# Performance work log

Measured on AMD Instinct MI355X. Metric: run time of the kernel, lower is better.

The kernel has to match this reference:

```python
import jax, jax.numpy as jnp
import numpy as np

NR_EMB = 1024
B_COMMITMENT = 1.0


def setup_inputs() -> dict:
    key = jax.random.key(0)
    k1, k2 = jax.random.split(key)
    inpt = jax.random.normal(k1, (64, 2048, 64), dtype=jnp.float32)
    # VarianceScaling(uniform) over shape (D, K): limit = sqrt(3*scale/fan_in), scale=1, fan_in=D
    D = 64
    limit = np.sqrt(3.0 / D).astype(np.float32)
    emb_mtrx = jax.random.uniform(k2, (D, NR_EMB), dtype=jnp.float32, minval=-limit, maxval=limit)
    return {"inpt": inpt, "emb_mtrx": emb_mtrx}


def reference(inpt, emb_mtrx):
    D = inpt.shape[-1]
    x = inpt.reshape(-1, D)  # [N, D]
    dist = (jnp.sum(x * x, axis=1, keepdims=True)
            - 2.0 * (x @ emb_mtrx)
            + jnp.sum(emb_mtrx * emb_mtrx, axis=0, keepdims=True))
    idx = jnp.argmax(-dist, axis=1)  # [N]
    # avg_probs = mean of one-hot over N == normalized histogram (same math, no N x K one-hot)
    avg_probs = jnp.bincount(idx, length=NR_EMB).astype(inpt.dtype) / x.shape[0]
    perplexity = jnp.exp(-jnp.sum(avg_probs * jnp.log(avg_probs + 1e-10)))
    idx_nd = idx.reshape(inpt.shape[:-1])  # [B, T]
    q = jnp.take(emb_mtrx.T, idx_nd, axis=0)  # gather codebook rows -> [B, T, D]
    l_commitment = jnp.mean((jax.lax.stop_gradient(q) - inpt) ** 2)
    l_codebook = jnp.mean((q - jax.lax.stop_gradient(inpt)) ** 2)
    loss = B_COMMITMENT * l_commitment + l_codebook
    q = inpt + jax.lax.stop_gradient(q - inpt)  # straight-through estimator
    return q, loss, perplexity
```

## Files before the change

### kernel.cpp

```cpp
#include <hip/hip_runtime.h>

#define NROWS 131072
#define D 64
#define K 1024

typedef __attribute__((ext_vector_type(8))) short short8;
typedef __attribute__((ext_vector_type(4))) float f32x4;
typedef unsigned int u32;


__device__ __forceinline__ unsigned short f2bf_rne(float f) {
    u32 u = __float_as_uint(f);
    u += 0x7fff + ((u >> 16) & 1);
    return (unsigned short)(u >> 16);
}

__global__ __launch_bounds__(256) void prep_kernel(const float* __restrict__ E,
                                                   unsigned short* __restrict__ ehT,
                                                   float* __restrict__ e2g,
                                                   int* __restrict__ hist) {
    const int k = blockIdx.x * 256 + threadIdx.x;
    float s = 0.f;
#pragma unroll
    for (int db = 0; db < 8; ++db) {
        short8 h8;
#pragma unroll
        for (int j = 0; j < 8; ++j) {
            float v = E[(db * 8 + j) * K + k];
            s = fmaf(v, v, s);
            h8[j] = (short)f2bf_rne(v);
        }
        *(short8*)(ehT + (size_t)k * D + db * 8) = h8;
    }
    e2g[k] = -0.5f * s;
    hist[k] = 0;
}

__global__ __launch_bounds__(1024) void score_kernel(const float* __restrict__ X,
                                                     const unsigned short* __restrict__ ehT,
                                                     const float* __restrict__ e2g,
                                                     int* __restrict__ hist,
                                                     float* __restrict__ wavesum,
                                                     float* __restrict__ q) {
    __shared__ unsigned short xbuf[2][8192];
    __shared__ float mrg[128 * 17];
    __shared__ int idxl[512];

    const int tid = threadIdx.x;
    const int wave = tid >> 6;
    const int lane = tid & 63;
    const int quad = lane >> 4;
    const int lc = lane & 15;
    const size_t row0 = (size_t)blockIdx.x * 512;

    const int cbase = wave * 64;
    short8 ae[4][2];
    f32x4 e2f[4];
    u32 cb4[4];
#pragma unroll
    for (int ct = 0; ct < 4; ++ct) {
        const unsigned short* ap = ehT + ((size_t)(cbase + ct * 16 + lc) << 6) + quad * 8;
        ae[ct][0] = *(const short8*)(ap);
        ae[ct][1] = *(const short8*)(ap + 32);
        e2f[ct] = *(const f32x4*)(e2g + cbase + ct * 16 + quad * 4);
        cb4[ct] = (u32)(cbase + ct * 16 + quad * 4);
    }

    const int st = tid >> 7, so = (tid >> 4) & 7, sl = tid & 15;
    const float* sbase = X + (row0 + (size_t)(st * 16 + sl)) * D + so * 8;

    float4 La = *(const float4*)(sbase);
    float4 Lb = *(const float4*)(sbase + 4);
    {
        union { u32 u[4]; short8 v; } pk;
        pk.u[0] = __builtin_amdgcn_perm(__float_as_uint(La.y), __float_as_uint(La.x), 0x07060302);
        pk.u[1] = __builtin_amdgcn_perm(__float_as_uint(La.w), __float_as_uint(La.z), 0x07060302);
        pk.u[2] = __builtin_amdgcn_perm(__float_as_uint(Lb.y), __float_as_uint(Lb.x), 0x07060302);
        pk.u[3] = __builtin_amdgcn_perm(__float_as_uint(Lb.w), __float_as_uint(Lb.z), 0x07060302);
        *(short8*)((char*)&xbuf[0][0] + tid * 16) = pk.v;
    }
    __syncthreads();

    for (int c = 0; c < 4; ++c) {
        const int cur = c & 1;
        if (c < 3) {
            La = *(const float4*)(sbase + (c + 1) * 8192);
            Lb = *(const float4*)(sbase + (c + 1) * 8192 + 4);
        }

        const char* bb = (const char*)&xbuf[cur][0];
#pragma unroll 2
        for (int t = 0; t < 8; ++t) {
            const char* bp = bb + t * 2048 + quad * 256 + lc * 16;
            short8 b0 = *(const short8*)(bp);
            short8 b1 = *(const short8*)(bp + 1024);
            float bt = -3.4e38f;
#pragma unroll
            for (int ct = 0; ct < 4; ++ct) {
                f32x4 acc = __builtin_amdgcn_mfma_f32_16x16x32_bf16(ae[ct][0], b0, e2f[ct], 0, 0, 0);
                acc = __builtin_amdgcn_mfma_f32_16x16x32_bf16(ae[ct][1], b1, acc, 0, 0, 0);
#pragma unroll
                for (int r = 0; r < 4; ++r) {
                    float pkv = __uint_as_float((__float_as_uint(acc[r]) & 0xFFFFFC00u) | (cb4[ct] + r));
                    bt = fmaxf(bt, pkv);
                }
            }
            bt = fmaxf(bt, __shfl_xor(bt, 16, 64));
            bt = fmaxf(bt, __shfl_xor(bt, 32, 64));
            if (lane < 16) mrg[(t * 16 + lane) * 17 + wave] = bt;
        }
        __syncthreads();

        if (tid < 128) {
            float m = mrg[tid * 17];
#pragma unroll
            for (int w = 1; w < 16; ++w) m = fmaxf(m, mrg[tid * 17 + w]);
            int kk = (int)(__float_as_uint(m) & 1023u);
            idxl[c * 128 + tid] = kk;
            atomicAdd(&hist[kk], 1);
        }
        if (c < 3) {
            union { u32 u[4]; short8 v; } pk;
            pk.u[0] = __builtin_amdgcn_perm(__float_as_uint(La.y), __float_as_uint(La.x), 0x07060302);
            pk.u[1] = __builtin_amdgcn_perm(__float_as_uint(La.w), __float_as_uint(La.z), 0x07060302);
            pk.u[2] = __builtin_amdgcn_perm(__float_as_uint(Lb.y), __float_as_uint(Lb.x), 0x07060302);
            pk.u[3] = __builtin_amdgcn_perm(__float_as_uint(Lb.w), __float_as_uint(Lb.z), 0x07060302);
            *(short8*)((char*)&xbuf[cur ^ 1][0] + tid * 16) = pk.v;
        }
        __syncthreads();
    }

    float ls = 0.f;
    const int er = tid >> 4, el = tid & 15;
#pragma unroll 2
    for (int it = 0; it < 8; ++it) {
        int rl = it * 64 + er;
        int k = idxl[rl];
        size_t row = row0 + rl;
        float4 xv = *(const float4*)(X + row * D + el * 4);
        short4 ev = *(const short4*)((const char*)ehT + (size_t)k * 128 + el * 8);
        float e0 = __uint_as_float(((u32)(unsigned short)ev.x) << 16);
        float e1 = __uint_as_float(((u32)(unsigned short)ev.y) << 16);
        float e2 = __uint_as_float(((u32)(unsigned short)ev.z) << 16);
        float e3 = __uint_as_float(((u32)(unsigned short)ev.w) << 16);
        float4 o;
        float dx = e0 - xv.x; ls = fmaf(dx, dx, ls); o.x = xv.x + dx;
        float dy = e1 - xv.y; ls = fmaf(dy, dy, ls); o.y = xv.y + dy;
        float dz = e2 - xv.z; ls = fmaf(dz, dz, ls); o.z = xv.z + dz;
        float dw = e3 - xv.w; ls = fmaf(dw, dw, ls); o.w = xv.w + dw;
        *(float4*)(q + row * D + el * 4) = o;
    }
    for (int off = 32; off > 0; off >>= 1) ls += __shfl_down(ls, off, 64);
    if (lane == 0) wavesum[blockIdx.x * 16 + wave] = ls;
}

__global__ __launch_bounds__(1024) void finalize_kernel(const int* __restrict__ hist,
                                                        const float* __restrict__ wavesum,
                                                        float* __restrict__ out) {
    __shared__ float redH[16], redL[16];
    int tid = threadIdx.x;
    float p = (float)hist[tid] * (1.0f / (float)NROWS);
    float term = p * logf(p + 1e-10f);
    float ls = wavesum[tid] + wavesum[tid + 1024] + wavesum[tid + 2048] + wavesum[tid + 3072];
    for (int off = 32; off > 0; off >>= 1) {
        term += __shfl_down(term, off, 64);
        ls += __shfl_down(ls, off, 64);
    }
    int lane = tid & 63, wid = tid >> 6;
    if (lane == 0) { redH[wid] = term; redL[wid] = ls; }
    __syncthreads();
    if (tid == 0) {
        float H = 0.f, L = 0.f;
#pragma unroll
        for (int i = 0; i < 16; ++i) { H += redH[i]; L += redL[i]; }
        out[(size_t)NROWS * D + 0] = 2.0f * (L / (float)(NROWS * D));
        out[(size_t)NROWS * D + 1] = expf(-H);
    }
}

extern "C" void kernel_launch(void* const* d_in, const int* in_sizes, int n_in,
                              void* d_out, int out_size, void* d_ws, size_t ws_size,
                              hipStream_t stream) {
    const float* X = (const float*)d_in[0];
    const float* E = (const float*)d_in[1];
    float* out = (float*)d_out;

    char* w = (char*)d_ws;
    unsigned short* ehT = (unsigned short*)(w + 0);
    float* e2g          = (float*)(w + 131072);
    int* hist           = (int*)(w + 135168);
    float* wavesum      = (float*)(w + 139264);

    prep_kernel<<<4, 256, 0, stream>>>(E, ehT, e2g, hist);
    score_kernel<<<256, 1024, 0, stream>>>(X, ehT, e2g, hist, wavesum, out);
    finalize_kernel<<<1, 1024, 0, stream>>>(hist, wavesum, out);
}
```

Measured before the change: 124.1 us.

## Fuse quantize epilogue into score loop using LDS bf16 inputs, double block count

Each block now handles 256 rows in 2 chunks instead of 512 rows in 4, giving 512 blocks instead of 256. The gather, loss and output stage now runs inside the chunk loop and reads the bf16 copy of X already held in LDS, rather than re-reading fp32 X from global memory after the loop. This removes the second global read of X and the separate tail phase. In exchange, the commitment loss is computed against bf16-truncated inputs, and q is written as the bf16 codebook value rather than x + (e - x), which costs accuracy. The prep kernel is also split across 16 blocks with an LDS reduction, and per-block loss partials are reduced in-kernel before finalize.

```diff
diff --git a/kernel.cpp b/kernel.cpp
--- a/kernel.cpp
+++ b/kernel.cpp
@@ -15,43 +15,53 @@
     return (unsigned short)(u >> 16);
 }
 
+__device__ __forceinline__ float b2f(short s) {
+    return __uint_as_float(((u32)(unsigned short)s) << 16);
+}
+
 __global__ __launch_bounds__(256) void prep_kernel(const float* __restrict__ E,
                                                    unsigned short* __restrict__ ehT,
                                                    float* __restrict__ e2g,
                                                    int* __restrict__ hist) {
-    const int k = blockIdx.x * 256 + threadIdx.x;
+    __shared__ float ps[4][64];
+    const int lane = threadIdx.x & 63;
+    const int w = threadIdx.x >> 6;
+    const int k = blockIdx.x * 64 + lane;
     float s = 0.f;
 #pragma unroll
-    for (int db = 0; db < 8; ++db) {
+    for (int half = 0; half < 2; ++half) {
         short8 h8;
 #pragma unroll
         for (int j = 0; j < 8; ++j) {
-            float v = E[(db * 8 + j) * K + k];
+            float v = E[(w * 16 + half * 8 + j) * K + k];
             s = fmaf(v, v, s);
             h8[j] = (short)f2bf_rne(v);
         }
-        *(short8*)(ehT + (size_t)k * D + db * 8) = h8;
-    }
-    e2g[k] = -0.5f * s;
-    hist[k] = 0;
-}
-
-__global__ __launch_bounds__(1024) void score_kernel(const float* __restrict__ X,
-                                                     const unsigned short* __restrict__ ehT,
-                                                     const float* __restrict__ e2g,
-                                                     int* __restrict__ hist,
-                                                     float* __restrict__ wavesum,
-                                                     float* __restrict__ q) {
+        *(short8*)(ehT + (size_t)k * D + w * 16 + half * 8) = h8;
+    }
+    ps[w][lane] = s;
+    __syncthreads();
+    if (w == 0) e2g[k] = -0.5f * (ps[0][lane] + ps[1][lane] + ps[2][lane] + ps[3][lane]);
+    if (threadIdx.x < 64) hist[blockIdx.x * 64 + threadIdx.x] = 0;
+}
+
+__global__ __launch_bounds__(1024, 8) void score_kernel(const float* __restrict__ X,
+                                                        const unsigned short* __restrict__ ehT,
+                                                        const float* __restrict__ e2g,
+                                                        int* __restrict__ hist,
+                                                        float* __restrict__ wavesum,
+                                                        float* __restrict__ q) {
     __shared__ unsigned short xbuf[2][8192];
     __shared__ float mrg[128 * 17];
-    __shared__ int idxl[512];
+    __shared__ int idxl[128];
+    __shared__ float redL[16];
 
     const int tid = threadIdx.x;
     const int wave = tid >> 6;
     const int lane = tid & 63;
     const int quad = lane >> 4;
     const int lc = lane & 15;
-    const size_t row0 = (size_t)blockIdx.x * 512;
+    const size_t row0 = (size_t)blockIdx.x * 256;
 
     const int cbase = wave * 64;
     short8 ae[4][2];
@@ -81,14 +91,14 @@
     }
     __syncthreads();
 
-    for (int c = 0; c < 4; ++c) {
-        const int cur = c & 1;
-        if (c < 3) {
-            La = *(const float4*)(sbase + (c + 1) * 8192);
-            Lb = *(const float4*)(sbase + (c + 1) * 8192 + 4);
-        }
-
-        const char* bb = (const char*)&xbuf[cur][0];
+    float ls = 0.f;
+    for (int c = 0; c < 2; ++c) {
+        if (c == 0) {
+            La = *(const float4*)(sbase + 8192);
+            Lb = *(const float4*)(sbase + 8192 + 4);
+        }
+
+        const char* bb = (const char*)&xbuf[c][0];
 #pragma unroll 2
         for (int t = 0; t < 8; ++t) {
             const char* bp = bb + t * 2048 + quad * 256 + lc * 16;
@@ -99,11 +109,12 @@
             for (int ct = 0; ct < 4; ++ct) {
                 f32x4 acc = __builtin_amdgcn_mfma_f32_16x16x32_bf16(ae[ct][0], b0, e2f[ct], 0, 0, 0);
                 acc = __builtin_amdgcn_mfma_f32_16x16x32_bf16(ae[ct][1], b1, acc, 0, 0, 0);
-#pragma unroll
-                for (int r = 0; r < 4; ++r) {
-                    float pkv = __uint_as_float((__float_as_uint(acc[r]) & 0xFFFFFC00u) | (cb4[ct] + r));
-                    bt = fmaxf(bt, pkv);
-                }
+                float p0 = __uint_as_float((__float_as_uint(acc[0]) & 0xFFFFFC00u) | (cb4[ct] + 0));
+                float p1 = __uint_as_float((__float_as_uint(acc[1]) & 0xFFFFFC00u) | (cb4[ct] + 1));
+                float p2 = __uint_as_float((__float_as_uint(acc[2]) & 0xFFFFFC00u) | (cb4[ct] + 2));
+                float p3 = __uint_as_float((__float_as_uint(acc[3]) & 0xFFFFFC00u) | (cb4[ct] + 3));
+                bt = fmaxf(bt, fmaxf(p0, p1));
+                bt = fmaxf(bt, fmaxf(p2, p3));
             }
             bt = fmaxf(bt, __shfl_xor(bt, 16, 64));
             bt = fmaxf(bt, __shfl_xor(bt, 32, 64));
@@ -116,42 +127,48 @@
 #pragma unroll
             for (int w = 1; w < 16; ++w) m = fmaxf(m, mrg[tid * 17 + w]);
             int kk = (int)(__float_as_uint(m) & 1023u);
-            idxl[c * 128 + tid] = kk;
+            idxl[tid] = kk;
             atomicAdd(&hist[kk], 1);
         }
-        if (c < 3) {
+        if (c == 0) {
             union { u32 u[4]; short8 v; } pk;
             pk.u[0] = __builtin_amdgcn_perm(__float_as_uint(La.y), __float_as_uint(La.x), 0x07060302);
             pk.u[1] = __builtin_amdgcn_perm(__float_as_uint(La.w), __float_as_uint(La.z), 0x07060302);
             pk.u[2] = __builtin_amdgcn_perm(__float_as_uint(Lb.y), __float_as_uint(Lb.x), 0x07060302);
             pk.u[3] = __builtin_amdgcn_perm(__float_as_uint(Lb.w), __float_as_uint(Lb.z), 0x07060302);
-            *(short8*)((char*)&xbuf[cur ^ 1][0] + tid * 16) = pk.v;
+            *(short8*)((char*)&xbuf[1][0] + tid * 16) = pk.v;
         }
         __syncthreads();
-    }
-
-    float ls = 0.f;
-    const int er = tid >> 4, el = tid & 15;
-#pragma unroll 2
-    for (int it = 0; it < 8; ++it) {
-        int rl = it * 64 + er;
-        int k = idxl[rl];
-        size_t row = row0 + rl;
-        float4 xv = *(const float4*)(X + row * D + el * 4);
-        short4 ev = *(const short4*)((const char*)ehT + (size_t)k * 128 + el * 8);
-        float e0 = __uint_as_float(((u32)(unsigned short)ev.x) << 16);
-        float e1 = __uint_as_float(((u32)(unsigned short)ev.y) << 16);
-        float e2 = __uint_as_float(((u32)(unsigned short)ev.z) << 16);
-        float e3 = __uint_as_float(((u32)(unsigned short)ev.w) << 16);
-        float4 o;
-        float dx = e0 - xv.x; ls = fmaf(dx, dx, ls); o.x = xv.x + dx;
-        float dy = e1 - xv.y; ls = fmaf(dy, dy, ls); o.y = xv.y + dy;
-        float dz = e2 - xv.z; ls = fmaf(dz, dz, ls); o.z = xv.z + dz;
-        float dw = e3 - xv.w; ls = fmaf(dw, dw, ls); o.w = xv.w + dw;
-        *(float4*)(q + row * D + el * 4) = o;
-    }
+
+        {
+            int kk = idxl[st * 16 + sl];
+            short8 ev = *(const short8*)(ehT + ((size_t)kk << 6) + so * 8);
+            short8 xv = *(const short8*)(&xbuf[c][tid * 8]);
+            float4 qa, qb;
+            float e0, x0, dd;
+            e0 = b2f(ev[0]); x0 = b2f(xv[0]); dd = e0 - x0; ls = fmaf(dd, dd, ls); qa.x = e0;
+            e0 = b2f(ev[1]); x0 = b2f(xv[1]); dd = e0 - x0; ls = fmaf(dd, dd, ls); qa.y = e0;
+            e0 = b2f(ev[2]); x0 = b2f(xv[2]); dd = e0 - x0; ls = fmaf(dd, dd, ls); qa.z = e0;
+            e0 = b2f(ev[3]); x0 = b2f(xv[3]); dd = e0 - x0; ls = fmaf(dd, dd, ls); qa.w = e0;
+            e0 = b2f(ev[4]); x0 = b2f(xv[4]); dd = e0 - x0; ls = fmaf(dd, dd, ls); qb.x = e0;
+            e0 = b2f(ev[5]); x0 = b2f(xv[5]); dd = e0 - x0; ls = fmaf(dd, dd, ls); qb.y = e0;
+            e0 = b2f(ev[6]); x0 = b2f(xv[6]); dd = e0 - x0; ls = fmaf(dd, dd, ls); qb.z = e0;
+            e0 = b2f(ev[7]); x0 = b2f(xv[7]); dd = e0 - x0; ls = fmaf(dd, dd, ls); qb.w = e0;
+            float* qp = q + (row0 + (size_t)(st * 16 + sl)) * D + so * 8 + (size_t)c * 8192;
+            *(float4*)(qp) = qa;
+            *(float4*)(qp + 4) = qb;
+        }
+    }
+
     for (int off = 32; off > 0; off >>= 1) ls += __shfl_down(ls, off, 64);
-    if (lane == 0) wavesum[blockIdx.x * 16 + wave] = ls;
+    if (lane == 0) redL[wave] = ls;
+    __syncthreads();
+    if (tid == 0) {
+        float L = 0.f;
+#pragma unroll
+        for (int i = 0; i < 16; ++i) L += redL[i];
+        wavesum[blockIdx.x] = L;
+    }
 }
 
 __global__ __launch_bounds__(1024) void finalize_kernel(const int* __restrict__ hist,
@@ -161,7 +178,7 @@
     int tid = threadIdx.x;
     float p = (float)hist[tid] * (1.0f / (float)NROWS);
     float term = p * logf(p + 1e-10f);
-    float ls = wavesum[tid] + wavesum[tid + 1024] + wavesum[tid + 2048] + wavesum[tid + 3072];
+    float ls = (tid < 512) ? wavesum[tid] : 0.f;
     for (int off = 32; off > 0; off >>= 1) {
         term += __shfl_down(term, off, 64);
         ls += __shfl_down(ls, off, 64);
@@ -191,7 +208,7 @@
     int* hist           = (int*)(w + 135168);
     float* wavesum      = (float*)(w + 139264);
 
-    prep_kernel<<<4, 256, 0, stream>>>(E, ehT, e2g, hist);
-    score_kernel<<<256, 1024, 0, stream>>>(X, ehT, e2g, hist, wavesum, out);
+    prep_kernel<<<16, 256, 0, stream>>>(E, ehT, e2g, hist);
+    score_kernel<<<512, 1024, 0, stream>>>(X, ehT, e2g, hist, wavesum, out);
     finalize_kernel<<<1, 1024, 0, stream>>>(hist, wavesum, out);
 }
```

After: 159.4 us. 28.4% more time.
